# Performance work log

Measured on AMD Instinct MI355X. Metric: run time of the kernel, lower is better.

Reference implementation:

```python
import jax, jax.numpy as jnp
import numpy as np

N = 512       # num_nodes (feature dim of x == num_nodes, per GCNConv(num_nodes, f1))
BZ = 32       # subjects
TC = 256      # tc_length
F1 = 256
F2 = 128
E = 524288    # edges in the given (corr) graph over all bz*N nodes
NTOT = BZ * N
SLOPE = 0.2   # leaky relu negative_slope


def setup_inputs() -> dict:
    key = jax.random.key(0)
    ks = jax.random.split(key, 17)
    w = lambda k, shape: (jax.random.normal(k, shape, jnp.float32) * (shape[-1] ** -0.5))
    return {
        "x": jax.random.normal(ks[0], (NTOT, N), jnp.float32),
        "t": jax.random.normal(ks[1], (NTOT, TC), jnp.float32),
        "gumbel_u": jax.random.uniform(ks[2], (BZ, N, N, 2), jnp.float32),
        "edge_index": jax.random.randint(ks[3], (2, E), 0, NTOT, jnp.int64 if jax.config.jax_enable_x64 else jnp.int32),
        "conv1_w": w(ks[4], (F1, N)),
        "conv1_b": jnp.zeros((F1,), jnp.float32),
        "conv2_w": w(ks[5], (F2, F1)),
        "conv2_b": jnp.zeros((F2,), jnp.float32),
        "fc_cat_w": w(ks[6], (2, 2 * TC)),
        "fc_cat_b": jnp.zeros((2,), jnp.float32),
        "fcn1_w": w(ks[7], (256, F2 * 2 * N)),
        "fcn1_b": jnp.zeros((256,), jnp.float32),
        "fcn2_w": w(ks[8], (32, 256)),
        "fcn2_b": jnp.zeros((32,), jnp.float32),
        "fcn3_w": w(ks[9], (2, 32)),
        "fcn3_b": jnp.zeros((2,), jnp.float32),
    }


def _gcn_dense(x, A, W, b):
    # PyG GCNConv on a dense 0/1 adjacency A (edge r->c means A[r,c]=1):
    # add self loop, in-degree symmetric norm, aggregate sources into targets.
    n = A.shape[0]
    Ah = A + jnp.eye(n, dtype=A.dtype)
    deg = Ah.sum(axis=0)                                  # in-degree (targets = cols)
    dis = jnp.where(deg > 0, jax.lax.rsqrt(deg), 0.0)
    M = dis[:, None] * Ah * dis[None, :]                  # M[j,i] = d_j^-1/2 A_hat[j,i] d_i^-1/2
    return M.T @ (x @ W.T) + b


def _gcn_sparse(x, row, col, W, b):
    n = x.shape[0]
    loops = jnp.arange(n, dtype=row.dtype)
    r = jnp.concatenate([row, loops])
    c = jnp.concatenate([col, loops])
    deg = jax.ops.segment_sum(jnp.ones_like(c, x.dtype), c, num_segments=n)
    dis = jnp.where(deg > 0, jax.lax.rsqrt(deg), 0.0)
    norm = dis[r] * dis[c]                                # [E+n]
    xw = x @ W.T                                          # [n, out]
    out = jax.ops.segment_sum(xw[r] * norm[:, None], c, num_segments=n)
    return out + b


def reference(x, t, gumbel_u, edge_index, conv1_w, conv1_b, conv2_w, conv2_b,
              fc_cat_w, fc_cat_b, fcn1_w, fcn1_b, fcn2_w, fcn2_b, fcn3_w, fcn3_b):
    bz = t.shape[0] // N
    tb = t.reshape(bz, N, -1)
    xb = x.reshape(bz, N, -1)
    # fc_cat(relu(cat([senders, receivers]))) factors into per-node terms:
    Ws = fc_cat_w[:, :TC]   # multiplies senders half
    Wr = fc_cat_w[:, TC:]   # multiplies receivers half

    def per_sample(ti, xi, ui):
        u = jax.nn.relu(ti)                               # [N, TC]
        ls = u @ Ws.T                                     # [N, 2] sender term
        lr = u @ Wr.T                                     # [N, 2] receiver term
        # pair k = i*N+j has receiver t_i, sender t_j
        logits = lr[:, None, :] + ls[None, :, :] + fc_cat_b   # [N, N, 2]
        g = -jnp.log(-jnp.log(jnp.clip(ui, 1e-9, 1.0 - 1e-9)))  # Gumbel(0,1)
        y = logits + g                                    # tau = 1
        A = (jnp.argmax(y, axis=-1) == 0).astype(xi.dtype)    # hard sample, class 0 => edge
        A = jax.lax.stop_gradient(A)                      # torch.where -> indices blocks grad
        h = jax.nn.relu(_gcn_dense(xi, A, conv1_w, conv1_b))
        return _gcn_dense(h, A, conv2_w, conv2_b)         # [N, F2]

    x_op = jax.vmap(per_sample)(tb, xb, gumbel_u)         # [bz, N, F2]

    row, col = edge_index[0], edge_index[1]
    x_corr = jax.nn.relu(_gcn_sparse(x, row, col, conv1_w, conv1_b))
    x_corr = _gcn_sparse(x_corr, row, col, conv2_w, conv2_b)   # [bz*N, F2]

    emb = jnp.concatenate([x_op.reshape(-1, F2), x_corr], axis=1)  # [bz*N, 2*F2]
    emb = emb.reshape(bz, -1)                             # [bz, 2*F2*N]
    h = jax.nn.leaky_relu(emb @ fcn1_w.T + fcn1_b, SLOPE)
    h = jax.nn.leaky_relu(h @ fcn2_w.T + fcn2_b, SLOPE)
    return h @ fcn3_w.T + fcn3_b                          # [bz, 2]
```

## Files before the change

### kernel.cpp

```cpp
#include <hip/hip_runtime.h>
#include <hip/hip_bf16.h>

typedef __bf16 bf16_t;
typedef __bf16 bf16x8 __attribute__((ext_vector_type(8)));
typedef __bf16 bf16x4 __attribute__((ext_vector_type(4)));
typedef float f32x4 __attribute__((ext_vector_type(4)));

constexpr int kN = 512;
constexpr int kBZ = 32;
constexpr int kTC = 256;
constexpr int kE = 524288;
constexpr int kNTOT = 16384;

__device__ __forceinline__ void gll16(const bf16_t* g, bf16_t* l) {
    __builtin_amdgcn_global_load_lds((const __attribute__((address_space(1))) void*)g,
                                     (__attribute__((address_space(3))) void*)l, 16, 0, 0);
}

__device__ __forceinline__ void stage128x64(const bf16_t* __restrict__ src, int ld,
                                            bf16_t* lds, int wave, int lane) {
#pragma unroll
    for (int i = 0; i < 4; i++) {
        int r0 = (wave * 4 + i) * 8;
        int r = r0 + (lane >> 3);
        int c = (lane & 7) ^ (r & 7);
        gll16(src + (size_t)r * ld + c * 8, lds + r0 * 64);
    }
}

__device__ __forceinline__ bf16x8 rdfrag(const bf16_t* lds, int row, int cc) {
    return *(const bf16x8*)(lds + row * 64 + ((cc ^ (row & 7)) * 8));
}

__global__ __launch_bounds__(256) void k_front(const float* __restrict__ c1w, const float* __restrict__ c2w,
                                               bf16_t* __restrict__ c1b, bf16_t* __restrict__ c2b,
                                               int* __restrict__ counts, float* __restrict__ degsum,
                                               const float* __restrict__ tin, const float* __restrict__ fcw,
                                               const float* __restrict__ fcb, float4* __restrict__ lsr) {
    int b = blockIdx.x;
    if (b < 192) {
        int i = b * 256 + threadIdx.x;
        const int n0 = 32768, n1 = n0 + 8192, n2 = n1 + 4096, n3 = n2 + 4096;
        if (i < n0) {
            float4 v = ((const float4*)c1w)[i];
            bf16x4 o = {(bf16_t)v.x, (bf16_t)v.y, (bf16_t)v.z, (bf16_t)v.w};
            ((bf16x4*)c1b)[i] = o;
        } else if (i < n1) {
            int j = i - n0;
            float4 v = ((const float4*)c2w)[j];
            bf16x4 o = {(bf16_t)v.x, (bf16_t)v.y, (bf16_t)v.z, (bf16_t)v.w};
            ((bf16x4*)c2b)[j] = o;
        } else if (i < n2) {
            ((int4*)counts)[i - n1] = make_int4(0, 0, 0, 0);
        } else if (i < n3) {
            ((float4*)degsum)[i - n2] = make_float4(0.f, 0.f, 0.f, 0.f);
        }
    } else {
        int row = (b - 192) * 4 + (threadIdx.x >> 6);
        int lane = threadIdx.x & 63;
        const float* tr = tin + (size_t)row * kTC;
        float s0 = 0, s1 = 0, r0 = 0, r1 = 0;
        for (int k = lane; k < kTC; k += 64) {
            float u = fmaxf(tr[k], 0.f);
            s0 += u * fcw[k];
            s1 += u * fcw[512 + k];
            r0 += u * fcw[256 + k];
            r1 += u * fcw[768 + k];
        }
#pragma unroll
        for (int off = 32; off > 0; off >>= 1) {
            s0 += __shfl_down(s0, off); s1 += __shfl_down(s1, off);
            r0 += __shfl_down(r0, off); r1 += __shfl_down(r1, off);
        }
        if (lane == 0) lsr[row] = make_float4(s0 + fcb[0], s1 + fcb[1], r0, r1);
    }
}

__global__ __launch_bounds__(256) void k_adj(const float* __restrict__ gum, const float4* __restrict__ lsr,
                                             bf16_t* __restrict__ AT, float* __restrict__ degsum) {
    int s = blockIdx.z;
    int a0 = blockIdx.y * 64, b0 = blockIdx.x * 64;
    __shared__ bf16_t tile[64][72];
    int t = threadIdx.x;
    int lb = t & 63, ra = t >> 6;
    int b = b0 + lb;
    float4 pb = lsr[s * kN + b];
#pragma unroll 4
    for (int p = 0; p < 16; p++) {
        int a = a0 + p * 4 + ra;
        float4 qa = lsr[s * kN + a];
        float2 gv = *(const float2*)(gum + ((((size_t)s * kN + a) * kN + b) << 1));
        float u0 = fmaxf(gv.x, 1e-9f);
        float u1 = fmaxf(gv.y, 1e-9f);
        float g0 = -__logf(-__logf(u0));
        float g1 = -__logf(-__logf(u1));
        float v = ((qa.z + pb.x + g0) >= (qa.w + pb.y + g1)) ? 1.f : 0.f;
        if (a == b) v += 1.f;
        tile[lb][p * 4 + ra] = (bf16_t)v;
    }
    __syncthreads();
    int rj = t >> 3, li = (t & 7) * 8;
#pragma unroll
    for (int p = 0; p < 2; p++) {
        int j = p * 32 + rj;
        bf16x8 v = *(const bf16x8*)&tile[j][li];
        *(bf16x8*)(AT + ((size_t)s * kN + b0 + j) * kN + a0 + li) = v;
        float ps = 0;
#pragma unroll
        for (int q = 0; q < 8; q++) ps += (float)v[q];
        ps += __shfl_down(ps, 4);
        ps += __shfl_down(ps, 2);
        ps += __shfl_down(ps, 1);
        if ((t & 7) == 0) atomicAdd(degsum + s * kN + b0 + j, ps);
    }
}

template <int MODE>
__global__ __launch_bounds__(256) void k_gemm(const bf16_t* __restrict__ A, const bf16_t* __restrict__ B,
                                              bf16_t* __restrict__ C, int K, int lda, int ldb, int ldc,
                                              size_t sA, size_t sB, size_t sC,
                                              const float* __restrict__ degsum, const float* __restrict__ bias) {
    int m0 = blockIdx.x * 128, n0 = blockIdx.y * 128, s = blockIdx.z;
    const bf16_t* Ab = A + sA * s + (size_t)m0 * lda;
    const bf16_t* Bb = B + sB * s + (size_t)n0 * ldb;
    C += sC * s;
    __shared__ __align__(16) bf16_t As[2][128 * 64], Bs[2][128 * 64];
    f32x4 acc[4][4] = {};
    int tid = threadIdx.x;
    int wave = tid >> 6, lane = tid & 63;
    int wm = (wave & 1) * 64, wn = (wave >> 1) * 64;
    int fm = lane & 15, fq = lane >> 4;
    stage128x64(Ab, lda, As[0], wave, lane);
    stage128x64(Bb, ldb, Bs[0], wave, lane);
    int cur = 0;
    for (int kb = 0;;) {
        int kn = kb + 64;
        __syncthreads();
        if (kn < K) {
            stage128x64(Ab + kn, lda, As[cur ^ 1], wave, lane);
            stage128x64(Bb + kn, ldb, Bs[cur ^ 1], wave, lane);
        }
#pragma unroll
        for (int kk = 0; kk < 2; kk++) {
            bf16x8 af[4], bfr[4];
#pragma unroll
            for (int i = 0; i < 4; i++) {
                af[i] = rdfrag(As[cur], wm + i * 16 + fm, kk * 4 + fq);
                bfr[i] = rdfrag(Bs[cur], wn + i * 16 + fm, kk * 4 + fq);
            }
#pragma unroll
            for (int i = 0; i < 4; i++)
#pragma unroll
                for (int j = 0; j < 4; j++)
                    acc[i][j] = __builtin_amdgcn_mfma_f32_16x16x32_bf16(af[i], bfr[j], acc[i][j], 0, 0, 0);
        }
        kb = kn;
        if (kb >= K) break;
        cur ^= 1;
    }
#pragma unroll
    for (int i = 0; i < 4; i++) {
#pragma unroll
        for (int r = 0; r < 4; r++) {
            int row = wm + i * 16 + fq * 4 + r;
            float sc = rsqrtf(degsum[(size_t)s * kN + m0 + row]);
#pragma unroll
            for (int j = 0; j < 4; j++) {
                int col = n0 + wn + j * 16 + fm;
                float v = sc * acc[i][j][r] + bias[col];
                if constexpr (MODE == 1) v = fmaxf(v, 0.f);
                C[(size_t)(m0 + row) * ldc + col] = (bf16_t)v;
            }
        }
    }
}

template <bool AF32, int F, int DENSE_ROWS>
__global__ __launch_bounds__(256) void k_gemmT(const void* __restrict__ Ap, const bf16_t* __restrict__ B,
                                               bf16_t* __restrict__ XW, bf16_t* __restrict__ ZT, int K,
                                               const float* __restrict__ degsum) {
    int m0 = blockIdx.x * 128, n0 = blockIdx.y * 128;
    constexpr int AST = AF32 ? 9216 : 8192;
    __shared__ __align__(16) bf16_t smem[2 * AST + 2 * 8192];
    bf16_t* A0 = smem;
    bf16_t* A1 = smem + AST;
    bf16_t* B0 = smem + 2 * AST;
    bf16_t* B1 = smem + 2 * AST + 8192;
    f32x4 acc[4][4] = {};
    int tid = threadIdx.x;
    int wave = tid >> 6, lane = tid & 63;
    int wm = (wave & 1) * 64, wn = (wave >> 1) * 64;
    int fm = lane & 15, fq = lane >> 4;
    int srow = tid >> 3, scol = (tid & 7) * 8;
    const float* Af = (const float*)Ap;
    const bf16_t* Abf = (const bf16_t*)Ap;
    if constexpr (AF32) {
#pragma unroll
        for (int p = 0; p < 4; p++) {
            int row = p * 32 + srow;
            const float* ap = Af + (size_t)(m0 + row) * K + scol;
            float4 lo = *(const float4*)ap, hi = *(const float4*)(ap + 4);
            bf16x8 o = {(bf16_t)lo.x, (bf16_t)lo.y, (bf16_t)lo.z, (bf16_t)lo.w,
                        (bf16_t)hi.x, (bf16_t)hi.y, (bf16_t)hi.z, (bf16_t)hi.w};
            *(bf16x8*)&A0[row * 72 + scol] = o;
        }
    } else {
        stage128x64(Abf + (size_t)m0 * K, K, A0, wave, lane);
    }
    stage128x64(B + (size_t)n0 * K, K, B0, wave, lane);
    int cur = 0;
    for (int kb = 0;;) {
        int kn = kb + 64;
        bool more = kn < K;
        bf16_t* Ac = cur ? A1 : A0;
        bf16_t* An = cur ? A0 : A1;
        bf16_t* Bc = cur ? B1 : B0;
        bf16_t* Bn = cur ? B0 : B1;
        float4 plo[4], phi[4];
        __syncthreads();
        if (more) {
            if constexpr (AF32) {
#pragma unroll
                for (int p = 0; p < 4; p++) {
                    int row = p * 32 + srow;
                    const float* ap = Af + (size_t)(m0 + row) * K + kn + scol;
                    plo[p] = *(const float4*)ap;
                    phi[p] = *(const float4*)(ap + 4);
                }
            } else {
                stage128x64(Abf + (size_t)m0 * K + kn, K, An, wave, lane);
            }
            stage128x64(B + (size_t)n0 * K + kn, K, Bn, wave, lane);
        }
#pragma unroll
        for (int kk = 0; kk < 2; kk++) {
            bf16x8 af[4], bfr[4];
#pragma unroll
            for (int i = 0; i < 4; i++) {
                if constexpr (AF32)
                    af[i] = *(const bf16x8*)&Ac[(wm + i * 16 + fm) * 72 + kk * 32 + fq * 8];
                else
                    af[i] = rdfrag(Ac, wm + i * 16 + fm, kk * 4 + fq);
                bfr[i] = rdfrag(Bc, wn + i * 16 + fm, kk * 4 + fq);
            }
#pragma unroll
            for (int i = 0; i < 4; i++)
#pragma unroll
                for (int j = 0; j < 4; j++)
                    acc[i][j] = __builtin_amdgcn_mfma_f32_16x16x32_bf16(af[i], bfr[j], acc[i][j], 0, 0, 0);
        }
        if constexpr (AF32) {
            if (more) {
#pragma unroll
                for (int p = 0; p < 4; p++) {
                    int row = p * 32 + srow;
                    bf16x8 o = {(bf16_t)plo[p].x, (bf16_t)plo[p].y, (bf16_t)plo[p].z, (bf16_t)plo[p].w,
                                (bf16_t)phi[p].x, (bf16_t)phi[p].y, (bf16_t)phi[p].z, (bf16_t)phi[p].w};
                    *(bf16x8*)&An[row * 72 + scol] = o;
                }
            }
        }
        kb = kn;
        if (kb >= K) break;
        cur ^= 1;
    }
    bool doT = (m0 < DENSE_ROWS);
    __syncthreads();
#pragma unroll
    for (int i = 0; i < 4; i++) {
#pragma unroll
        for (int r = 0; r < 4; r++) {
            int row = wm + i * 16 + fq * 4 + r;
            float sc = doT ? rsqrtf(degsum[m0 + row]) : 0.f;
#pragma unroll
            for (int j = 0; j < 4; j++) {
                int col = wn + j * 16 + fm;
                float v = acc[i][j][r];
                XW[(size_t)(m0 + row) * F + n0 + col] = (bf16_t)v;
                if (doT) smem[col * 136 + row] = (bf16_t)(sc * v);
            }
        }
    }
    if (doT) {
        __syncthreads();
        int fr = tid >> 1, hi = (tid & 1) * 64;
        bf16_t* zrow = ZT + ((size_t)(m0 >> 9) * F + n0 + fr) * kN + (m0 & 511) + hi;
#pragma unroll
        for (int q = 0; q < 8; q++)
            *(bf16x8*)(zrow + q * 8) = *(const bf16x8*)&smem[fr * 136 + hi + q * 8];
    }
}


__global__ __launch_bounds__(256) void k_hist(const int* __restrict__ col, int* __restrict__ counts) {
    int e = blockIdx.x * 256 + threadIdx.x;
    if (e < kE) atomicAdd(&counts[col[e]], 1);
}

__global__ __launch_bounds__(1024) void k_scan(const int* __restrict__ counts, int* __restrict__ offsets,
                                               int* __restrict__ cursor, float* __restrict__ dis_s) {
    __shared__ int ldc_[16896];
    __shared__ int sums[1024];
    int t = threadIdx.x;
#define IDX(j) ((j) + ((j) >> 5))
    for (int i = 0; i < 16; i++) {
        int g = i * 1024 + t;
        int c = counts[g];
        ldc_[IDX(g)] = c;
        dis_s[g] = rsqrtf((float)(c + 1));
    }
    __syncthreads();
    int s = 0;
    for (int i = 0; i < 16; i++) s += ldc_[IDX(t * 16 + i)];
    sums[t] = s;
    __syncthreads();
    for (int off = 1; off < 1024; off <<= 1) {
        int y = (t >= off) ? sums[t - off] : 0;
        __syncthreads();
        sums[t] += y;
        __syncthreads();
    }
    int run = sums[t] - s;
    for (int i = 0; i < 16; i++) {
        int j = t * 16 + i;
        int c = ldc_[IDX(j)];
        ldc_[IDX(j)] = run;
        run += c;
    }
    __syncthreads();
    for (int i = 0; i < 16; i++) {
        int g = i * 1024 + t;
        int o = ldc_[IDX(g)];
        offsets[g] = o;
        cursor[g] = o;
    }
#undef IDX
}

__global__ __launch_bounds__(256) void k_fill(const int* __restrict__ row, const int* __restrict__ col,
                                              int* __restrict__ cursor, int* __restrict__ list) {
    int e = blockIdx.x * 256 + threadIdx.x;
    if (e < kE) {
        int p = atomicAdd(&cursor[col[e]], 1);
        list[p] = row[e];
    }
}

template <int F, bool RELU>
__global__ __launch_bounds__(256) void k_sagg(const bf16_t* __restrict__ XW, int rowOffIn,
                                              const int* __restrict__ list, const int* __restrict__ offsets,
                                              const int* __restrict__ counts, const float* __restrict__ dis_s,
                                              const float* __restrict__ bias, bf16_t* __restrict__ OUT,
                                              int outColOff) {
    constexpr int TPR = F / 8;
    constexpr int RPB = 256 / TPR;
    int j = blockIdx.x * RPB + threadIdx.x / TPR;
    int f8 = (threadIdx.x % TPR) * 8;
    float dj = dis_s[j];
    const bf16_t* base = XW + (size_t)rowOffIn * F;
    float acc[8];
    {
        bf16x8 v = *(const bf16x8*)(base + (size_t)j * F + f8);
#pragma unroll
        for (int q = 0; q < 8; q++) acc[q] = dj * (float)v[q];
    }
    int off = offsets[j], cnt = counts[j];
    int e = 0;
    int nb = cnt & ~7;
    if (nb) {
        int r[8];
#pragma unroll
        for (int q = 0; q < 8; q++) r[q] = list[off + q];
        while (true) {
            int en = e + 8;
            bool more = en < nb;
            int rn[8];
            if (more) {
#pragma unroll
                for (int q = 0; q < 8; q++) rn[q] = list[off + en + q];
            }
            float d[8];
#pragma unroll
            for (int q = 0; q < 8; q++) d[q] = dis_s[r[q]];
            bf16x8 v0 = *(const bf16x8*)(base + (size_t)r[0] * F + f8);
            bf16x8 v1 = *(const bf16x8*)(base + (size_t)r[1] * F + f8);
            bf16x8 v2 = *(const bf16x8*)(base + (size_t)r[2] * F + f8);
            bf16x8 v3 = *(const bf16x8*)(base + (size_t)r[3] * F + f8);
            bf16x8 v4 = *(const bf16x8*)(base + (size_t)r[4] * F + f8);
            bf16x8 v5 = *(const bf16x8*)(base + (size_t)r[5] * F + f8);
            bf16x8 v6 = *(const bf16x8*)(base + (size_t)r[6] * F + f8);
            bf16x8 v7 = *(const bf16x8*)(base + (size_t)r[7] * F + f8);
#pragma unroll
            for (int q = 0; q < 8; q++)
                acc[q] += ((d[0] * (float)v0[q] + d[1] * (float)v1[q]) + (d[2] * (float)v2[q] + d[3] * (float)v3[q])) +
                          ((d[4] * (float)v4[q] + d[5] * (float)v5[q]) + (d[6] * (float)v6[q] + d[7] * (float)v7[q]));
            e = en;
            if (!more) break;
#pragma unroll
            for (int q = 0; q < 8; q++) r[q] = rn[q];
        }
    }
    for (; e + 4 <= cnt; e += 4) {
        int r0 = list[off + e], r1 = list[off + e + 1], r2 = list[off + e + 2], r3 = list[off + e + 3];
        float d0 = dis_s[r0], d1 = dis_s[r1], d2 = dis_s[r2], d3 = dis_s[r3];
        bf16x8 v0 = *(const bf16x8*)(base + (size_t)r0 * F + f8);
        bf16x8 v1 = *(const bf16x8*)(base + (size_t)r1 * F + f8);
        bf16x8 v2 = *(const bf16x8*)(base + (size_t)r2 * F + f8);
        bf16x8 v3 = *(const bf16x8*)(base + (size_t)r3 * F + f8);
#pragma unroll
        for (int q = 0; q < 8; q++)
            acc[q] += (d0 * (float)v0[q] + d1 * (float)v1[q]) + (d2 * (float)v2[q] + d3 * (float)v3[q]);
    }
    for (; e < cnt; e++) {
        int r = list[off + e];
        float d = dis_s[r];
        bf16x8 v = *(const bf16x8*)(base + (size_t)r * F + f8);
#pragma unroll
        for (int q = 0; q < 8; q++) acc[q] += d * (float)v[q];
    }
    bf16x8 o;
#pragma unroll
    for (int q = 0; q < 8; q++) {
        float v = dj * acc[q] + bias[f8 + q];
        if (RELU) v = fmaxf(v, 0.f);
        o[q] = (bf16_t)v;
    }
    *(bf16x8*)(OUT + (size_t)j * 256 + outColOff + f8) = o;
}

__global__ __launch_bounds__(256) void k_fcn1(const bf16_t* __restrict__ EMB, const float* __restrict__ W1,
                                              float* __restrict__ partials) {
    int tid = threadIdx.x, wave = tid >> 6, lane = tid & 63;
    int fm = lane & 15, fq = lane >> 4;
    int kb0 = blockIdx.x * 512;
    f32x4 acc[2][4] = {};
#pragma unroll 4
    for (int ks = 0; ks < 512; ks += 32) {
        int k = kb0 + ks + fq * 8;
        bf16x8 a0 = *(const bf16x8*)(EMB + (size_t)fm * 131072 + k);
        bf16x8 a1 = *(const bf16x8*)(EMB + (size_t)(16 + fm) * 131072 + k);
        bf16x8 bfr[4];
#pragma unroll
        for (int j = 0; j < 4; j++) {
            int n = wave * 64 + j * 16 + fm;
            const float* p = W1 + (size_t)n * 131072 + k;
            float4 lo = *(const float4*)p;
            float4 hi = *(const float4*)(p + 4);
            bf16x8 b = {(bf16_t)lo.x, (bf16_t)lo.y, (bf16_t)lo.z, (bf16_t)lo.w,
                        (bf16_t)hi.x, (bf16_t)hi.y, (bf16_t)hi.z, (bf16_t)hi.w};
            bfr[j] = b;
        }
#pragma unroll
        for (int j = 0; j < 4; j++) {
            acc[0][j] = __builtin_amdgcn_mfma_f32_16x16x32_bf16(a0, bfr[j], acc[0][j], 0, 0, 0);
            acc[1][j] = __builtin_amdgcn_mfma_f32_16x16x32_bf16(a1, bfr[j], acc[1][j], 0, 0, 0);
        }
    }
    float* P = partials + (size_t)blockIdx.x * 8192;
#pragma unroll
    for (int i = 0; i < 2; i++)
#pragma unroll
        for (int j = 0; j < 4; j++)
#pragma unroll
            for (int r = 0; r < 4; r++)
                P[(size_t)(i * 16 + fq * 4 + r) * 256 + wave * 64 + j * 16 + fm] = acc[i][j][r];
}

__global__ __launch_bounds__(256) void k_reduce(const float* __restrict__ partials, float* __restrict__ h1pre) {
    int e = blockIdx.x * 256 + threadIdx.x;
    float s = 0;
#pragma unroll 8
    for (int i = 0; i < 256; i++) s += partials[(size_t)i * 8192 + e];
    h1pre[e] = s;
}

__global__ __launch_bounds__(256) void k_head(const float* __restrict__ h1pre, const float* __restrict__ b1,
                                              const float* __restrict__ W2, const float* __restrict__ b2,
                                              const float* __restrict__ W3, const float* __restrict__ b3,
                                              float* __restrict__ out) {
    __shared__ float h1s[32][256];
    __shared__ float h2s[32][32];
    int t = threadIdx.x;
    for (int i = 0; i < 32; i++) {
        float s = h1pre[i * 256 + t] + b1[t];
        h1s[i][t] = (s > 0.f) ? s : 0.2f * s;
    }
    __syncthreads();
    for (int p = 0; p < 4; p++) {
        int id = p * 256 + t, si = id >> 5, o2 = id & 31;
        float s = 0;
        for (int k = 0; k < 256; k++) s += h1s[si][k] * W2[o2 * 256 + k];
        s += b2[o2];
        h2s[si][o2] = (s > 0.f) ? s : 0.2f * s;
    }
    __syncthreads();
    if (t < 64) {
        int si = t >> 1, o3 = t & 1;
        float s = 0;
#pragma unroll
        for (int k = 0; k < 32; k++) s += h2s[si][k] * W3[o3 * 32 + k];
        out[si * 2 + o3] = s + b3[o3];
    }
}


extern "C" void kernel_launch(void* const* d_in, const int* in_sizes, int n_in,
                              void* d_out, int out_size, void* d_ws, size_t ws_size,
                              hipStream_t stream) {
    const float* x = (const float*)d_in[0];
    const float* t = (const float*)d_in[1];
    const float* gum = (const float*)d_in[2];
    const int* eidx = (const int*)d_in[3];
    const float* c1w = (const float*)d_in[4];
    const float* c1b = (const float*)d_in[5];
    const float* c2w = (const float*)d_in[6];
    const float* c2b = (const float*)d_in[7];
    const float* fcw = (const float*)d_in[8];
    const float* fcb = (const float*)d_in[9];
    const float* w1 = (const float*)d_in[10];
    const float* b1 = (const float*)d_in[11];
    const float* w2 = (const float*)d_in[12];
    const float* b2 = (const float*)d_in[13];
    const float* w3 = (const float*)d_in[14];
    const float* b3 = (const float*)d_in[15];
    float* out = (float*)d_out;
    (void)in_sizes; (void)n_in; (void)out_size; (void)ws_size;

    char* ws = (char*)d_ws;
    size_t off = 0;
    auto alloc = [&](size_t bytes) -> char* {
        char* p = ws + off;
        off += (bytes + 255) & ~size_t(255);
        return p;
    };
    bf16_t* c1wb = (bf16_t*)alloc((size_t)256 * 512 * 2);
    bf16_t* c2wb = (bf16_t*)alloc((size_t)128 * 256 * 2);
    float4* lsr = (float4*)alloc((size_t)kNTOT * 16);
    bf16_t* AT = (bf16_t*)alloc((size_t)kBZ * kN * kN * 2);
    float* degsum = (float*)alloc((size_t)kNTOT * 4);
    bf16_t* XW1_EMB = (bf16_t*)alloc((size_t)kNTOT * 256 * 2);
    bf16_t* Z1T = (bf16_t*)alloc((size_t)kBZ * 256 * 512 * 2);
    bf16_t* H = (bf16_t*)alloc((size_t)32768 * 256 * 2);
    bf16_t* XW2 = (bf16_t*)alloc((size_t)32768 * 128 * 2);
    bf16_t* Z2T = (bf16_t*)alloc((size_t)kBZ * 128 * 512 * 2);
    int* counts = (int*)alloc((size_t)kNTOT * 4);
    int* offsets = (int*)alloc((size_t)kNTOT * 4);
    int* cursor = (int*)alloc((size_t)kNTOT * 4);
    float* diss = (float*)alloc((size_t)kNTOT * 4);
    int* list = (int*)alloc((size_t)kE * 4);
    float* partials = (float*)alloc((size_t)256 * 8192 * 4);
    float* h1pre = (float*)alloc((size_t)8192 * 4);

    bf16_t* XW1 = XW1_EMB;
    bf16_t* EMB = XW1_EMB;

    k_front<<<4288, 256, 0, stream>>>(c1w, c2w, c1wb, c2wb, counts, degsum, t, fcw, fcb, lsr);
    k_adj<<<dim3(8, 8, 32), 256, 0, stream>>>(gum, lsr, AT, degsum);
    k_hist<<<2048, 256, 0, stream>>>(eidx + kE, counts);
    k_scan<<<1, 1024, 0, stream>>>(counts, offsets, cursor, diss);
    k_fill<<<2048, 256, 0, stream>>>(eidx, eidx + kE, cursor, list);
    k_gemmT<true, 256, kNTOT><<<dim3(128, 2, 1), 256, 0, stream>>>(x, c1wb, XW1, Z1T, 512, degsum);
    k_gemm<1><<<dim3(4, 2, 32), 256, 0, stream>>>(AT, Z1T, H, 512, 512, 512, 256,
                                                  (size_t)512 * 512, (size_t)256 * 512, (size_t)512 * 256,
                                                  degsum, c1b);
    k_sagg<256, true><<<2048, 256, 0, stream>>>(XW1, 0, list, offsets, counts, diss, c1b,
                                                H + (size_t)16384 * 256, 0);
    k_gemmT<false, 128, kNTOT><<<dim3(256, 1, 1), 256, 0, stream>>>(H, c2wb, XW2, Z2T, 256, degsum);
    k_gemm<2><<<dim3(4, 1, 32), 256, 0, stream>>>(AT, Z2T, EMB, 512, 512, 512, 256,
                                                  (size_t)512 * 512, (size_t)128 * 512, (size_t)512 * 256,
                                                  degsum, c2b);
    k_sagg<128, false><<<1024, 256, 0, stream>>>(XW2, 16384, list, offsets, counts, diss, c2b, EMB, 128);
    k_fcn1<<<256, 256, 0, stream>>>(EMB, w1, partials);
    k_reduce<<<32, 256, 0, stream>>>(partials, h1pre);
    k_head<<<1, 256, 0, stream>>>(h1pre, b1, w2, b2, w3, b3, out);
}
```

Measured before the change: 506.1 us.

## Fuse histogram into adjacency kernel, remap GEMM grids, and widen partials reduce

```diff
diff --git a/kernel.cpp b/kernel.cpp
--- a/kernel.cpp
+++ b/kernel.cpp
@@ -76,10 +76,17 @@
     }
 }
 
-__global__ __launch_bounds__(256) void k_adj(const float* __restrict__ gum, const float4* __restrict__ lsr,
-                                             bf16_t* __restrict__ AT, float* __restrict__ degsum) {
-    int s = blockIdx.z;
-    int a0 = blockIdx.y * 64, b0 = blockIdx.x * 64;
+__global__ __launch_bounds__(256) void k_adjhist(const float* __restrict__ gum, const float4* __restrict__ lsr,
+                                                 bf16_t* __restrict__ AT, float* __restrict__ degsum,
+                                                 const int* __restrict__ col, int* __restrict__ counts) {
+    int blk = blockIdx.x;
+    if (blk >= 2048) {
+        int e = (blk - 2048) * 256 + threadIdx.x;
+        if (e < kE) atomicAdd(&counts[col[e]], 1);
+        return;
+    }
+    int s = blk >> 6;
+    int a0 = ((blk >> 3) & 7) * 64, b0 = (blk & 7) * 64;
     __shared__ bf16_t tile[64][72];
     int t = threadIdx.x;
     int lb = t & 63, ra = t >> 6;
@@ -115,12 +122,26 @@
     }
 }
 
-template <int MODE>
+template <int MODE, int GDEC>
 __global__ __launch_bounds__(256) void k_gemm(const bf16_t* __restrict__ A, const bf16_t* __restrict__ B,
                                               bf16_t* __restrict__ C, int K, int lda, int ldb, int ldc,
                                               size_t sA, size_t sB, size_t sC,
                                               const float* __restrict__ degsum, const float* __restrict__ bias) {
-    int m0 = blockIdx.x * 128, n0 = blockIdx.y * 128, s = blockIdx.z;
+    int m0, n0, s;
+    {
+        int f = blockIdx.x;
+        if constexpr (GDEC == 1) {
+            int p = ((f >> 4) << 3) | (f & 7);
+            int y = (f >> 3) & 1;
+            s = p >> 2;
+            m0 = (p & 3) * 128;
+            n0 = y * 128;
+        } else {
+            s = ((f >> 5) << 3) | (f & 7);
+            m0 = ((f >> 3) & 3) * 128;
+            n0 = 0;
+        }
+    }
     const bf16_t* Ab = A + sA * s + (size_t)m0 * lda;
     const bf16_t* Bb = B + sB * s + (size_t)n0 * ldb;
     C += sC * s;
@@ -175,11 +196,19 @@
     }
 }
 
-template <bool AF32, int F, int DENSE_ROWS>
+template <bool AF32, int F, int DENSE_ROWS, bool PAIRXY>
 __global__ __launch_bounds__(256) void k_gemmT(const void* __restrict__ Ap, const bf16_t* __restrict__ B,
                                                bf16_t* __restrict__ XW, bf16_t* __restrict__ ZT, int K,
                                                const float* __restrict__ degsum) {
-    int m0 = blockIdx.x * 128, n0 = blockIdx.y * 128;
+    int m0, n0;
+    if constexpr (PAIRXY) {
+        int f = blockIdx.x;
+        m0 = (((f >> 4) << 3) | (f & 7)) * 128;
+        n0 = ((f >> 3) & 1) * 128;
+    } else {
+        m0 = blockIdx.x * 128;
+        n0 = blockIdx.y * 128;
+    }
     constexpr int AST = AF32 ? 9216 : 8192;
     __shared__ __align__(16) bf16_t smem[2 * AST + 2 * 8192];
     bf16_t* A0 = smem;
@@ -292,11 +321,6 @@
 }
 
 
-__global__ __launch_bounds__(256) void k_hist(const int* __restrict__ col, int* __restrict__ counts) {
-    int e = blockIdx.x * 256 + threadIdx.x;
-    if (e < kE) atomicAdd(&counts[col[e]], 1);
-}
-
 __global__ __launch_bounds__(1024) void k_scan(const int* __restrict__ counts, int* __restrict__ offsets,
                                                int* __restrict__ cursor, float* __restrict__ dis_s) {
     __shared__ int ldc_[16896];
@@ -467,11 +491,21 @@
 }
 
 __global__ __launch_bounds__(256) void k_reduce(const float* __restrict__ partials, float* __restrict__ h1pre) {
-    int e = blockIdx.x * 256 + threadIdx.x;
+    __shared__ float red[8][32];
+    int t = threadIdx.x;
+    int el = t & 31, q = t >> 5;
+    int e = blockIdx.x * 32 + el;
     float s = 0;
 #pragma unroll 8
-    for (int i = 0; i < 256; i++) s += partials[(size_t)i * 8192 + e];
-    h1pre[e] = s;
+    for (int i = 0; i < 32; i++) s += partials[(size_t)(q * 32 + i) * 8192 + e];
+    red[q][el] = s;
+    __syncthreads();
+    if (t < 32) {
+        float r = 0;
+#pragma unroll
+        for (int qq = 0; qq < 8; qq++) r += red[qq][t];
+        h1pre[blockIdx.x * 32 + t] = r;
+    }
 }
 
 __global__ __launch_bounds__(256) void k_head(const float* __restrict__ h1pre, const float* __restrict__ b1,
@@ -555,22 +589,21 @@
     bf16_t* EMB = XW1_EMB;
 
     k_front<<<4288, 256, 0, stream>>>(c1w, c2w, c1wb, c2wb, counts, degsum, t, fcw, fcb, lsr);
-    k_adj<<<dim3(8, 8, 32), 256, 0, stream>>>(gum, lsr, AT, degsum);
-    k_hist<<<2048, 256, 0, stream>>>(eidx + kE, counts);
+    k_adjhist<<<4096, 256, 0, stream>>>(gum, lsr, AT, degsum, eidx + kE, counts);
     k_scan<<<1, 1024, 0, stream>>>(counts, offsets, cursor, diss);
     k_fill<<<2048, 256, 0, stream>>>(eidx, eidx + kE, cursor, list);
-    k_gemmT<true, 256, kNTOT><<<dim3(128, 2, 1), 256, 0, stream>>>(x, c1wb, XW1, Z1T, 512, degsum);
-    k_gemm<1><<<dim3(4, 2, 32), 256, 0, stream>>>(AT, Z1T, H, 512, 512, 512, 256,
-                                                  (size_t)512 * 512, (size_t)256 * 512, (size_t)512 * 256,
-                                                  degsum, c1b);
+    k_gemmT<true, 256, kNTOT, true><<<256, 256, 0, stream>>>(x, c1wb, XW1, Z1T, 512, degsum);
+    k_gemm<1, 1><<<256, 256, 0, stream>>>(AT, Z1T, H, 512, 512, 512, 256,
+                                          (size_t)512 * 512, (size_t)256 * 512, (size_t)512 * 256,
+                                          degsum, c1b);
     k_sagg<256, true><<<2048, 256, 0, stream>>>(XW1, 0, list, offsets, counts, diss, c1b,
                                                 H + (size_t)16384 * 256, 0);
-    k_gemmT<false, 128, kNTOT><<<dim3(256, 1, 1), 256, 0, stream>>>(H, c2wb, XW2, Z2T, 256, degsum);
-    k_gemm<2><<<dim3(4, 1, 32), 256, 0, stream>>>(AT, Z2T, EMB, 512, 512, 512, 256,
-                                                  (size_t)512 * 512, (size_t)128 * 512, (size_t)512 * 256,
-                                                  degsum, c2b);
+    k_gemmT<false, 128, kNTOT, false><<<dim3(256, 1, 1), 256, 0, stream>>>(H, c2wb, XW2, Z2T, 256, degsum);
+    k_gemm<2, 2><<<128, 256, 0, stream>>>(AT, Z2T, EMB, 512, 512, 512, 256,
+                                          (size_t)512 * 512, (size_t)128 * 512, (size_t)512 * 256,
+                                          degsum, c2b);
     k_sagg<128, false><<<1024, 256, 0, stream>>>(XW2, 16384, list, offsets, counts, diss, c2b, EMB, 128);
     k_fcn1<<<256, 256, 0, stream>>>(EMB, w1, partials);
-    k_reduce<<<32, 256, 0, stream>>>(partials, h1pre);
+    k_reduce<<<256, 256, 0, stream>>>(partials, h1pre);
     k_head<<<1, 256, 0, stream>>>(h1pre, b1, w2, b2, w3, b3, out);
 }
```

New measurement: 484.7 us. 1.04x faster.
